# Kernel optimization log

Measured on AMD Instinct MI355X. Metric: run time of the kernel, lower is better.

The kernel has to match this reference:

```python
import jax, jax.numpy as jnp
import numpy as np

NUM_HEADS = 32
NUM_KV_HEADS = 8
HEAD_DIM = 128
ROPE_BASE = 10000.0


def rotate_half(x):
    half = x.shape[-1] // 2
    x1, x2 = x[..., :half], x[..., half:]
    return jnp.concatenate((-x2, x1), axis=-1)


def rope_cos_sin(position_ids, head_dim, dtype):
    # inv_freq: [head_dim/2]
    inv_freq = 1.0 / (ROPE_BASE ** (jnp.arange(0, head_dim, 2, dtype=jnp.float32) / head_dim))
    freqs = position_ids.astype(jnp.float32)[..., None] * inv_freq  # [B, S, hd/2]
    emb = jnp.concatenate((freqs, freqs), axis=-1)                  # [B, S, hd]
    # add head axis -> [B, 1, S, hd]
    return jnp.cos(emb)[:, None].astype(dtype), jnp.sin(emb)[:, None].astype(dtype)


def setup_inputs() -> dict:
    key = jax.random.key(0)
    k_x, k_q, k_k, k_v, k_o = jax.random.split(key, 5)
    B, S, H = 1, 2048, 4096
    w_scale = 0.02
    return {
        "hidden_states": jax.random.normal(k_x, (B, S, H), dtype=jnp.float32),
        "position_ids": jnp.broadcast_to(jnp.arange(S, dtype=jnp.int32), (B, S)),
        "Wq": jax.random.normal(k_q, (NUM_HEADS * HEAD_DIM, H), dtype=jnp.float32) * w_scale,
        "Wk": jax.random.normal(k_k, (NUM_KV_HEADS * HEAD_DIM, H), dtype=jnp.float32) * w_scale,
        "Wv": jax.random.normal(k_v, (NUM_KV_HEADS * HEAD_DIM, H), dtype=jnp.float32) * w_scale,
        "Wo": jax.random.normal(k_o, (H, NUM_HEADS * HEAD_DIM), dtype=jnp.float32) * w_scale,
    }


def reference(hidden_states, position_ids, Wq, Wk, Wv, Wo):
    B, S, H = hidden_states.shape
    n_rep = NUM_HEADS // NUM_KV_HEADS

    # projections (torch Linear: y = x @ W.T), reshape to [B, heads, S, hd]
    q = (hidden_states @ Wq.T).reshape(B, S, NUM_HEADS, HEAD_DIM).transpose(0, 2, 1, 3)
    k = (hidden_states @ Wk.T).reshape(B, S, NUM_KV_HEADS, HEAD_DIM).transpose(0, 2, 1, 3)
    v = (hidden_states @ Wv.T).reshape(B, S, NUM_KV_HEADS, HEAD_DIM).transpose(0, 2, 1, 3)

    cos, sin = rope_cos_sin(position_ids, HEAD_DIM, hidden_states.dtype)
    q = q * cos + rotate_half(q) * sin
    k = k * cos + rotate_half(k) * sin

    # repeat_kv: GQA expansion to [B, NUM_HEADS, S, hd]
    k = jnp.repeat(k, n_rep, axis=1)
    v = jnp.repeat(v, n_rep, axis=1)

    scale = 1.0 / jnp.sqrt(jnp.asarray(HEAD_DIM, dtype=hidden_states.dtype))
    scores = jnp.einsum('bhqd,bhkd->bhqk', q, k) * scale  # [B, H, S, S]

    # causal additive mask
    causal = jnp.tril(jnp.ones((S, S), dtype=bool))
    scores = jnp.where(causal[None, None], scores, jnp.finfo(scores.dtype).min)

    probs = jax.nn.softmax(scores, axis=-1)
    attn = jnp.einsum('bhqk,bhkd->bhqd', probs, v)         # [B, H, S, hd]
    attn = attn.transpose(0, 2, 1, 3).reshape(B, S, NUM_HEADS * HEAD_DIM)
    return attn @ Wo.T
```

## Files before the change

kernel.cpp:

```cpp
#include <hip/hip_runtime.h>
#include <hip/hip_bf16.h>
#include <stdint.h>

typedef __bf16 bf16;
typedef __attribute__((ext_vector_type(8))) __bf16 bf16x8;
typedef __attribute__((ext_vector_type(4))) __bf16 bf16x4;
typedef __attribute__((ext_vector_type(4))) float f32x4;
typedef __attribute__((ext_vector_type(16))) float f32x16;
typedef __attribute__((ext_vector_type(4))) unsigned int uint4v;

#define S_LEN 2048
#define HDIM  4096
#define NQH   32
#define NKVH  8
#define DHEAD 128
#define QKVN  6144
#define KOFF  4096
#define VOFF  5120
#define NSPLIT 4

__device__ __forceinline__ void gload_lds16(const bf16* g, bf16* l) {
  __builtin_amdgcn_global_load_lds(
      (const __attribute__((address_space(1))) unsigned int*)g,
      (__attribute__((address_space(3))) unsigned int*)l, 16, 0, 0);
}

__global__ __launch_bounds__(256) void cvt_f32_bf16(const float* __restrict__ in,
                                                    bf16* __restrict__ out, int n4) {
  int i = blockIdx.x * 256 + threadIdx.x;
  if (i >= n4) return;
  float4 v = ((const float4*)in)[i];
  bf16x4 ov = {(bf16)v.x, (bf16)v.y, (bf16)v.z, (bf16)v.w};
  *(bf16x4*)&out[(size_t)i * 4] = ov;
}

__global__ __launch_bounds__(256) void rope_table(const int* __restrict__ pos,
                                                  float* __restrict__ tab) {
  int idx = blockIdx.x * 256 + threadIdx.x;
  int i = idx & 63, s = idx >> 6;
  float p = (float)pos[s];
  float invf = powf(10000.0f, -(float)i * (1.0f / 64.0f));
  float ang = p * invf;
  tab[idx * 2]     = cosf(ang);
  tab[idx * 2 + 1] = sinf(ang);
}

__global__ __launch_bounds__(256) void rope_apply(bf16* __restrict__ QKV,
                                                  const float* __restrict__ tab) {
  int idx = blockIdx.x * 256 + threadIdx.x;
  int dp = idx & 63;
  int t = idx >> 6;
  int head = t % 40;
  int s = t / 40;
  float c  = tab[(s * 64 + dp) * 2];
  float sn = tab[(s * 64 + dp) * 2 + 1];
  size_t base = (size_t)s * QKVN + head * DHEAD;
  float x0 = (float)QKV[base + dp];
  float x1 = (float)QKV[base + 64 + dp];
  QKV[base + dp]      = (bf16)(x0 * c - x1 * sn);
  QKV[base + 64 + dp] = (bf16)(x1 * c + x0 * sn);
}

__global__ __launch_bounds__(256) void transpose_v(const bf16* __restrict__ QKV,
                                                   bf16* __restrict__ Vt) {
  __shared__ bf16 t[64][72];
  int tid = threadIdx.x;
  int bs = blockIdx.x * 64, bc = blockIdx.y * 64;
  int sl = tid >> 3, cb = (tid & 7) * 8;
#pragma unroll
  for (int ss = 0; ss < 64; ss += 32) {
    int s = sl + ss;
    *(bf16x8*)&t[s][cb] = *(const bf16x8*)&QKV[(size_t)(bs + s) * QKVN + VOFF + bc + cb];
  }
  __syncthreads();
  int cl = tid >> 3, sb = (tid & 7) * 8;
#pragma unroll
  for (int cc = 0; cc < 64; cc += 32) {
    int c = cl + cc;
    bf16x8 v;
#pragma unroll
    for (int k = 0; k < 8; ++k) v[k] = t[sb + k][c];
    *(bf16x8*)&Vt[(size_t)(bc + c) * S_LEN + bs + sb] = v;
  }
}

template <typename OutT>
__global__ __launch_bounds__(256) void gemm_bt(const bf16* __restrict__ A,
                                               const bf16* __restrict__ B,
                                               OutT* __restrict__ C,
                                               int M, int N, int K) {
  __shared__ bf16 At[128 * 64];
  __shared__ bf16 Bt[128 * 64];
  const int tid = threadIdx.x;
  const int w = tid >> 6, lane = tid & 63;
  const int r = lane & 15, g = lane >> 4;
  const int bm = blockIdx.y * 128, bn = blockIdx.x * 128;
  const int wm = (w >> 1) * 64, wn = (w & 1) * 64;
  f32x4 acc[4][4];
#pragma unroll
  for (int i = 0; i < 4; ++i)
#pragma unroll
    for (int j = 0; j < 4; ++j) acc[i][j] = (f32x4){0.f, 0.f, 0.f, 0.f};

  const int chunk0 = w * 256 + lane;

  for (int k0 = 0; k0 < K; k0 += 64) {
#pragma unroll
    for (int i = 0; i < 4; ++i) {
      int chunk = chunk0 + i * 64;
      int row = chunk >> 3, c8 = chunk & 7;
      int cs = ((c8 ^ (row & 7)) << 3) + k0;
      gload_lds16(&A[(size_t)(bm + row) * K + cs], &At[(w * 4 + i) * 512]);
      gload_lds16(&B[(size_t)(bn + row) * K + cs], &Bt[(w * 4 + i) * 512]);
    }
    __syncthreads();
#pragma unroll
    for (int ks = 0; ks < 2; ++ks) {
      bf16x8 af[4], bfr[4];
#pragma unroll
      for (int mi = 0; mi < 4; ++mi) {
        int row = wm + mi * 16 + r;
        af[mi] = *(const bf16x8*)&At[row * 64 + ((((ks << 2) + g) ^ (row & 7)) << 3)];
      }
#pragma unroll
      for (int nj = 0; nj < 4; ++nj) {
        int row = wn + nj * 16 + r;
        bfr[nj] = *(const bf16x8*)&Bt[row * 64 + ((((ks << 2) + g) ^ (row & 7)) << 3)];
      }
#pragma unroll
      for (int mi = 0; mi < 4; ++mi)
#pragma unroll
        for (int nj = 0; nj < 4; ++nj)
          acc[mi][nj] = __builtin_amdgcn_mfma_f32_16x16x32_bf16(af[mi], bfr[nj],
                                                                acc[mi][nj], 0, 0, 0);
    }
    __syncthreads();
  }
#pragma unroll
  for (int mi = 0; mi < 4; ++mi)
#pragma unroll
    for (int nj = 0; nj < 4; ++nj)
#pragma unroll
      for (int j = 0; j < 4; ++j) {
        int row = bm + wm + mi * 16 + g * 4 + j;
        int col = bn + wn + nj * 16 + r;
        C[(size_t)row * N + col] = (OutT)acc[mi][nj][j];
      }
}

__global__ __launch_bounds__(256) void attn_kernel(const bf16* __restrict__ QKV,
                                                   const bf16* __restrict__ Vt,
                                                   bf16* __restrict__ Opart,
                                                   float* __restrict__ Mpart,
                                                   float* __restrict__ Lpart) {
  __shared__ bf16 Kl[3][32 * 128];
  __shared__ bf16 Vl[3][128 * 32];
  const int tid = threadIdx.x;
  const int w = tid >> 6, lane = tid & 63;
  const int l31 = lane & 31, hi = lane >> 5;
  const int bx = blockIdx.x;
  const int kvh = bx & 7;
  const int rest = bx >> 3;
  const int s = rest & 3;
  const int qblk = 63 - (rest >> 2);
  const int h = kvh * 4 + w;
  const int q0 = qblk * 32;
  const int pid = (h * 64 + qblk) * NSPLIT + s;
  const float scale = 0.12751746f;

  const int nt = qblk + 1;
  const int t0 = (nt * s) >> 2;
  const int t1 = (nt * (s + 1)) >> 2;

  f32x16 o[4];
#pragma unroll
  for (int t = 0; t < 4; ++t)
#pragma unroll
    for (int r = 0; r < 16; ++r) o[t][r] = 0.f;
  float m_run = -1e30f, l_run = 0.f;

  auto stage = [&](int bufi, int kv0) {
#pragma unroll
    for (int ii = 0; ii < 2; ++ii) {
      int ins = w * 2 + ii;
      int hr = ins * 8 + (lane >> 3);
      int kvrow = hr >> 1, hK = hr & 1;
      int gk = ((lane & 7) ^ (kvrow & 7)) + 8 * hK;
      gload_lds16(&QKV[(size_t)(kv0 + kvrow) * QKVN + KOFF + kvh * DHEAD + gk * 8],
                  &Kl[bufi][ins * 512]);
      int pr = ins * 8 + (lane >> 3);
      int xv = (lane & 7) ^ (pr & 7);
      int dV = pr * 2 + (xv >> 2);
      gload_lds16(&Vt[(size_t)(kvh * DHEAD + dV) * S_LEN + kv0 + (xv & 3) * 8],
                  &Vl[bufi][ins * 512]);
    }
  };

  if (t0 < t1) {
    bf16x8 qf[8];
#pragma unroll
    for (int k8 = 0; k8 < 8; ++k8) {
      bf16x8 raw = *(const bf16x8*)&QKV[(size_t)(q0 + l31) * QKVN + h * DHEAD + k8 * 16 + hi * 8];
#pragma unroll
      for (int e = 0; e < 8; ++e) qf[k8][e] = (bf16)((float)raw[e] * scale);
    }

    int cur = t0 % 3;
    stage(cur, t0 * 32);
    if (t0 + 1 < t1) {
      stage(cur == 2 ? 0 : cur + 1, (t0 + 1) * 32);
      asm volatile("s_waitcnt vmcnt(4)" ::: "memory");
    } else {
      asm volatile("s_waitcnt vmcnt(0)" ::: "memory");
    }
    __builtin_amdgcn_s_barrier();
    asm volatile("" ::: "memory");

    for (int t = t0; t < t1; ++t) {
      if (t + 2 < t1) {
        int s2 = cur ? cur - 1 : 2;
        stage(s2, (t + 2) * 32);
      }

      f32x16 st;
#pragma unroll
      for (int r = 0; r < 16; ++r) st[r] = 0.f;
      __builtin_amdgcn_s_setprio(1);
#pragma unroll
      for (int k8 = 0; k8 < 8; ++k8) {
        int g = 2 * k8 + hi;
        bf16x8 kf = *(const bf16x8*)&Kl[cur][l31 * 128 + (g >> 3) * 64 +
                                             (((g & 7) ^ (l31 & 7)) << 3)];
        st = __builtin_amdgcn_mfma_f32_32x32x16_bf16(kf, qf[k8], st, 0, 0, 0);
      }
      __builtin_amdgcn_s_setprio(0);

      if (t == nt - 1) {
#pragma unroll
        for (int r = 0; r < 16; ++r) {
          int kvr = (r & 3) + 8 * (r >> 2) + 4 * hi;
          if (kvr > l31) st[r] = -1e30f;
        }
      }
      float pmax = st[0];
#pragma unroll
      for (int r = 1; r < 16; ++r) pmax = fmaxf(pmax, st[r]);
      pmax = fmaxf(pmax, __shfl_xor(pmax, 32));
      if (!__all(pmax - m_run <= 8.0f)) {
        float mnew = fmaxf(m_run, pmax);
        float corr = exp2f(m_run - mnew);
        m_run = mnew;
        l_run *= corr;
#pragma unroll
        for (int r = 0; r < 16; ++r) {
          float cr = __shfl(corr, (r & 3) + 8 * (r >> 2) + 4 * hi);
          o[0][r] *= cr; o[1][r] *= cr; o[2][r] *= cr; o[3][r] *= cr;
        }
      }
      float rs = 0.f;
#pragma unroll
      for (int r = 0; r < 16; ++r) { st[r] = exp2f(st[r] - m_run); rs += st[r]; }
      rs += __shfl_xor(rs, 32);
      l_run += rs;
      bf16x8 pf0, pf1;
      {
        unsigned int A0[4], X0[4];
#pragma unroll
        for (int j = 0; j < 4; ++j) {
          unsigned short lo = __builtin_bit_cast(unsigned short, (bf16)st[2 * j]);
          unsigned short hi16 = __builtin_bit_cast(unsigned short, (bf16)st[2 * j + 1]);
          A0[j] = (unsigned int)lo | ((unsigned int)hi16 << 16);
        }
#pragma unroll
        for (int j = 0; j < 4; ++j) X0[j] = __shfl_xor(A0[j], 32);
        uint4v w0v = {hi ? X0[2] : A0[0], hi ? X0[3] : A0[1],
                      hi ? A0[2] : X0[0], hi ? A0[3] : X0[1]};
        pf0 = __builtin_bit_cast(bf16x8, w0v);
      }
      {
        unsigned int A1[4], X1[4];
#pragma unroll
        for (int j = 0; j < 4; ++j) {
          unsigned short lo = __builtin_bit_cast(unsigned short, (bf16)st[8 + 2 * j]);
          unsigned short hi16 = __builtin_bit_cast(unsigned short, (bf16)st[9 + 2 * j]);
          A1[j] = (unsigned int)lo | ((unsigned int)hi16 << 16);
        }
#pragma unroll
        for (int j = 0; j < 4; ++j) X1[j] = __shfl_xor(A1[j], 32);
        uint4v w1v = {hi ? X1[2] : A1[0], hi ? X1[3] : A1[1],
                      hi ? A1[2] : X1[0], hi ? A1[3] : X1[1]};
        pf1 = __builtin_bit_cast(bf16x8, w1v);
      }
      __builtin_amdgcn_s_setprio(1);
#pragma unroll
      for (int tt = 0; tt < 4; ++tt) {
        int pr = tt * 16 + (l31 >> 1);
        int sb4 = (l31 & 1) << 2;
        bf16x8 v0 = *(const bf16x8*)&Vl[cur][pr * 64 + (((sb4 + hi) ^ (pr & 7)) << 3)];
        bf16x8 v1 = *(const bf16x8*)&Vl[cur][pr * 64 + (((sb4 + 2 + hi) ^ (pr & 7)) << 3)];
        o[tt] = __builtin_amdgcn_mfma_f32_32x32x16_bf16(pf0, v0, o[tt], 0, 0, 0);
        o[tt] = __builtin_amdgcn_mfma_f32_32x32x16_bf16(pf1, v1, o[tt], 0, 0, 0);
      }
      __builtin_amdgcn_s_setprio(0);

      if (t + 2 < t1) {
        asm volatile("s_waitcnt vmcnt(4)" ::: "memory");
      } else {
        asm volatile("s_waitcnt vmcnt(0)" ::: "memory");
      }
      __builtin_amdgcn_s_barrier();
      asm volatile("" ::: "memory");
      cur = (cur == 2) ? 0 : cur + 1;
    }
  }

  float linv = (l_run > 0.f) ? 1.0f / l_run : 0.f;
  if (hi == 0) {
    Mpart[pid * 32 + l31] = m_run;
    Lpart[pid * 32 + l31] = l_run;
  }
#pragma unroll
  for (int r = 0; r < 16; ++r) {
    int qloc = (r & 3) + 8 * (r >> 2) + 4 * hi;
    float li = __shfl(linv, qloc);
    size_t row = (size_t)pid * (32 * DHEAD) + (size_t)qloc * DHEAD;
#pragma unroll
    for (int t2 = 0; t2 < 4; ++t2)
      Opart[row + t2 * 32 + l31] = (bf16)(o[t2][r] * li);
  }
}

__global__ __launch_bounds__(256) void attn_merge(const bf16* __restrict__ Opart,
                                                  const float* __restrict__ Mpart,
                                                  const float* __restrict__ Lpart,
                                                  bf16* __restrict__ Oout) {
  const int bx = blockIdx.x;
  const int h = bx >> 6, qblk = bx & 63;
  const int tid = threadIdx.x;
  const int r = tid >> 3, cseg = (tid & 7) * 16;
  const int pid0 = bx * NSPLIT;
  float m[NSPLIT], l[NSPLIT];
  float M = -1e30f;
#pragma unroll
  for (int s = 0; s < NSPLIT; ++s) {
    m[s] = Mpart[(pid0 + s) * 32 + r];
    l[s] = Lpart[(pid0 + s) * 32 + r];
    M = fmaxf(M, m[s]);
  }
  float wsum = 0.f, wv[NSPLIT];
#pragma unroll
  for (int s = 0; s < NSPLIT; ++s) { wv[s] = l[s] * exp2f(m[s] - M); wsum += wv[s]; }
  float inv = 1.0f / wsum;
#pragma unroll
  for (int s = 0; s < NSPLIT; ++s) wv[s] *= inv;
  size_t dst = (size_t)(qblk * 32 + r) * HDIM + h * DHEAD + cseg;
#pragma unroll
  for (int half = 0; half < 2; ++half) {
    float acc[8];
#pragma unroll
    for (int e = 0; e < 8; ++e) acc[e] = 0.f;
#pragma unroll
    for (int s = 0; s < NSPLIT; ++s) {
      bf16x8 a = *(const bf16x8*)&Opart[(size_t)(pid0 + s) * (32 * DHEAD) +
                                        (size_t)r * DHEAD + cseg + half * 8];
#pragma unroll
      for (int e = 0; e < 8; ++e) acc[e] += wv[s] * (float)a[e];
    }
    bf16x8 out;
#pragma unroll
    for (int e = 0; e < 8; ++e) out[e] = (bf16)acc[e];
    *(bf16x8*)&Oout[dst + half * 8] = out;
  }
}

extern "C" void kernel_launch(void* const* d_in, const int* in_sizes, int n_in,
                              void* d_out, int out_size, void* d_ws, size_t ws_size,
                              hipStream_t stream) {
  const float* X   = (const float*)d_in[0];
  const int*   pos = (const int*)d_in[1];
  const float* Wq  = (const float*)d_in[2];
  const float* Wk  = (const float*)d_in[3];
  const float* Wv  = (const float*)d_in[4];
  const float* Wo  = (const float*)d_in[5];
  float* out = (float*)d_out;
  char* ws = (char*)d_ws;

  size_t off = 0;
  bf16* Xb    = (bf16*)(ws + off); off += (size_t)2048 * 4096 * 2;
  bf16* Wqkvb = (bf16*)(ws + off); off += (size_t)6144 * 4096 * 2;
  bf16* Wob   = (bf16*)(ws + off); off += (size_t)4096 * 4096 * 2;
  bf16* QKV   = (bf16*)(ws + off); off += (size_t)2048 * 6144 * 2;
  bf16* Vt    = (bf16*)(ws + off); off += (size_t)1024 * 2048 * 2;
  bf16* attnb = (bf16*)(ws + off); off += (size_t)2048 * 4096 * 2;
  float* tab  = (float*)(ws + off); off += (size_t)2048 * 64 * 2 * 4;
  float* Mpart = (float*)(ws + off); off += (size_t)8192 * 32 * 4;
  float* Lpart = (float*)(ws + off); off += (size_t)8192 * 32 * 4;

  bf16* Opart = (bf16*)Xb;

  cvt_f32_bf16<<<2048 * 4096 / 4 / 256, 256, 0, stream>>>(X, Xb, 2048 * 4096 / 4);
  cvt_f32_bf16<<<4096 * 4096 / 4 / 256, 256, 0, stream>>>(Wq, Wqkvb, 4096 * 4096 / 4);
  cvt_f32_bf16<<<1024 * 4096 / 4 / 256, 256, 0, stream>>>(Wk, Wqkvb + (size_t)4096 * 4096,
                                                          1024 * 4096 / 4);
  cvt_f32_bf16<<<1024 * 4096 / 4 / 256, 256, 0, stream>>>(Wv, Wqkvb + (size_t)5120 * 4096,
                                                          1024 * 4096 / 4);
  cvt_f32_bf16<<<4096 * 4096 / 4 / 256, 256, 0, stream>>>(Wo, Wob, 4096 * 4096 / 4);
  rope_table<<<2048 * 64 / 256, 256, 0, stream>>>(pos, tab);
  gemm_bt<bf16><<<dim3(QKVN / 128, 2048 / 128), 256, 0, stream>>>(Xb, Wqkvb, QKV,
                                                                  2048, QKVN, 4096);
  rope_apply<<<2048 * 40 * 64 / 256, 256, 0, stream>>>(QKV, tab);
  transpose_v<<<dim3(2048 / 64, 1024 / 64), 256, 0, stream>>>(QKV, Vt);
  attn_kernel<<<2048, 256, 0, stream>>>(QKV, Vt, Opart, Mpart, Lpart);
  attn_merge<<<2048, 256, 0, stream>>>(Opart, Mpart, Lpart, attnb);
  gemm_bt<float><<<dim3(4096 / 128, 2048 / 128), 256, 0, stream>>>(attnb, Wob, out,
                                                                   2048, 4096, 4096);
}
```

Baseline: 372.4 us.

## Replace GEMM with 256x256 double-buffered tiles, 8 waves, and XCD-aware swizzle

Both projection GEMMs move from 128x128 tiles with 4 waves to 256x256 tiles with 8 waves. The new kernel double-buffers LDS with async global-to-LDS prefetch of the next K slice, interleaved with MFMA phases and s_setprio hints. Block IDs are remapped so consecutive blocks spread across the 8 XCDs. Bigger tiles raise arithmetic intensity and the prefetch hides load latency. In exchange the grid is only 192 or 128 blocks for 256 CUs, which may underfill the GPU, and 128KB of LDS per block limits occupancy.

New measurement: 502.7 us. 1.35x slower.

```diff
diff --git a/kernel.cpp b/kernel.cpp
--- a/kernel.cpp
+++ b/kernel.cpp
@@ -85,65 +85,152 @@
 }
 
 template <typename OutT>
-__global__ __launch_bounds__(256) void gemm_bt(const bf16* __restrict__ A,
-                                               const bf16* __restrict__ B,
-                                               OutT* __restrict__ C,
-                                               int M, int N, int K) {
-  __shared__ bf16 At[128 * 64];
-  __shared__ bf16 Bt[128 * 64];
+__global__ __launch_bounds__(512, 2) void gemm_bt256(const bf16* __restrict__ A,
+                                                     const bf16* __restrict__ B,
+                                                     OutT* __restrict__ C,
+                                                     int M, int N, int K, int NX) {
+  __shared__ bf16 Al[2][256 * 64];
+  __shared__ bf16 Bl[2][256 * 64];
   const int tid = threadIdx.x;
   const int w = tid >> 6, lane = tid & 63;
   const int r = lane & 15, g = lane >> 4;
-  const int bm = blockIdx.y * 128, bn = blockIdx.x * 128;
-  const int wm = (w >> 1) * 64, wn = (w & 1) * 64;
-  f32x4 acc[4][4];
-#pragma unroll
-  for (int i = 0; i < 4; ++i)
-#pragma unroll
-    for (int j = 0; j < 4; ++j) acc[i][j] = (f32x4){0.f, 0.f, 0.f, 0.f};
-
-  const int chunk0 = w * 256 + lane;
-
-  for (int k0 = 0; k0 < K; k0 += 64) {
-#pragma unroll
-    for (int i = 0; i < 4; ++i) {
-      int chunk = chunk0 + i * 64;
-      int row = chunk >> 3, c8 = chunk & 7;
-      int cs = ((c8 ^ (row & 7)) << 3) + k0;
-      gload_lds16(&A[(size_t)(bm + row) * K + cs], &At[(w * 4 + i) * 512]);
-      gload_lds16(&B[(size_t)(bn + row) * K + cs], &Bt[(w * 4 + i) * 512]);
-    }
+  const int wr = w >> 2, wc = w & 3;
+  const int nwg = gridDim.x;
+  const int id = blockIdx.x;
+  const int q = nwg >> 3;
+  const int sw = (id & 7) * q + (id >> 3);
+  const int by = sw / NX, bx = sw - by * NX;
+  const int bm = by * 256, bn = bx * 256;
+
+  f32x4 acc[8][4];
+#pragma unroll
+  for (int mi = 0; mi < 8; ++mi)
+#pragma unroll
+    for (int nj = 0; nj < 4; ++nj) acc[mi][nj] = (f32x4){0.f, 0.f, 0.f, 0.f};
+
+  int rowS[4], colS[4];
+#pragma unroll
+  for (int i = 0; i < 4; ++i) {
+    int chunk = (i * 8 + w) * 64 + lane;
+    rowS[i] = chunk >> 3;
+    colS[i] = ((chunk & 7) ^ (rowS[i] & 7)) << 3;
+  }
+
+  const int NT = K >> 6;
+#pragma unroll
+  for (int i = 0; i < 4; ++i) {
+    gload_lds16(&A[(size_t)(bm + rowS[i]) * K + colS[i]], &Al[0][(i * 8 + w) * 512]);
+    gload_lds16(&B[(size_t)(bn + rowS[i]) * K + colS[i]], &Bl[0][(i * 8 + w) * 512]);
+  }
+  __syncthreads();
+
+  for (int t = 0; t < NT; ++t) {
+    const int cur = t & 1;
+    const bf16* Ac = Al[cur];
+    const bf16* Bc = Bl[cur];
+    bf16* An = Al[cur ^ 1];
+    bf16* Bn = Bl[cur ^ 1];
+    const int kn = (t + 1) << 6;
+    const bool pre = (t + 1 < NT);
+    bf16x8 af[4], bfr[4];
+
+    if (pre) {
+#pragma unroll
+      for (int i = 0; i < 4; ++i)
+        gload_lds16(&A[(size_t)(bm + rowS[i]) * K + kn + colS[i]], &An[(i * 8 + w) * 512]);
+    }
+#pragma unroll
+    for (int mi = 0; mi < 4; ++mi) {
+      int row = wr * 128 + mi * 16 + r;
+      af[mi] = *(const bf16x8*)&Ac[row * 64 + ((g ^ (row & 7)) << 3)];
+    }
+#pragma unroll
+    for (int nj = 0; nj < 4; ++nj) {
+      int row = wc * 64 + nj * 16 + r;
+      bfr[nj] = *(const bf16x8*)&Bc[row * 64 + ((g ^ (row & 7)) << 3)];
+    }
+    __builtin_amdgcn_s_barrier();
+    asm volatile("s_waitcnt lgkmcnt(0)" ::: "memory");
+    __builtin_amdgcn_s_setprio(1);
+#pragma unroll
+    for (int mi = 0; mi < 4; ++mi)
+#pragma unroll
+      for (int nj = 0; nj < 4; ++nj)
+        acc[mi][nj] = __builtin_amdgcn_mfma_f32_16x16x32_bf16(af[mi], bfr[nj],
+                                                              acc[mi][nj], 0, 0, 0);
+    __builtin_amdgcn_s_setprio(0);
+    __builtin_amdgcn_s_barrier();
+
+    if (pre) {
+#pragma unroll
+      for (int i = 0; i < 4; ++i)
+        gload_lds16(&B[(size_t)(bn + rowS[i]) * K + kn + colS[i]], &Bn[(i * 8 + w) * 512]);
+    }
+#pragma unroll
+    for (int mi = 0; mi < 4; ++mi) {
+      int row = wr * 128 + (mi + 4) * 16 + r;
+      af[mi] = *(const bf16x8*)&Ac[row * 64 + ((g ^ (row & 7)) << 3)];
+    }
+    __builtin_amdgcn_s_barrier();
+    asm volatile("s_waitcnt lgkmcnt(0)" ::: "memory");
+    __builtin_amdgcn_s_setprio(1);
+#pragma unroll
+    for (int mi = 0; mi < 4; ++mi)
+#pragma unroll
+      for (int nj = 0; nj < 4; ++nj)
+        acc[mi + 4][nj] = __builtin_amdgcn_mfma_f32_16x16x32_bf16(af[mi], bfr[nj],
+                                                                  acc[mi + 4][nj], 0, 0, 0);
+    __builtin_amdgcn_s_setprio(0);
+    __builtin_amdgcn_s_barrier();
+
+#pragma unroll
+    for (int mi = 0; mi < 4; ++mi) {
+      int row = wr * 128 + mi * 16 + r;
+      af[mi] = *(const bf16x8*)&Ac[row * 64 + (((4 + g) ^ (row & 7)) << 3)];
+    }
+#pragma unroll
+    for (int nj = 0; nj < 4; ++nj) {
+      int row = wc * 64 + nj * 16 + r;
+      bfr[nj] = *(const bf16x8*)&Bc[row * 64 + (((4 + g) ^ (row & 7)) << 3)];
+    }
+    __builtin_amdgcn_s_barrier();
+    asm volatile("s_waitcnt lgkmcnt(0)" ::: "memory");
+    __builtin_amdgcn_s_setprio(1);
+#pragma unroll
+    for (int mi = 0; mi < 4; ++mi)
+#pragma unroll
+      for (int nj = 0; nj < 4; ++nj)
+        acc[mi][nj] = __builtin_amdgcn_mfma_f32_16x16x32_bf16(af[mi], bfr[nj],
+                                                              acc[mi][nj], 0, 0, 0);
+    __builtin_amdgcn_s_setprio(0);
+    __builtin_amdgcn_s_barrier();
+
+#pragma unroll
+    for (int mi = 0; mi < 4; ++mi) {
+      int row = wr * 128 + (mi + 4) * 16 + r;
+      af[mi] = *(const bf16x8*)&Ac[row * 64 + (((4 + g) ^ (row & 7)) << 3)];
+    }
+    __builtin_amdgcn_s_barrier();
+    asm volatile("s_waitcnt lgkmcnt(0)" ::: "memory");
+    __builtin_amdgcn_s_setprio(1);
+#pragma unroll
+    for (int mi = 0; mi < 4; ++mi)
+#pragma unroll
+      for (int nj = 0; nj < 4; ++nj)
+        acc[mi + 4][nj] = __builtin_amdgcn_mfma_f32_16x16x32_bf16(af[mi], bfr[nj],
+                                                                  acc[mi + 4][nj], 0, 0, 0);
+    __builtin_amdgcn_s_setprio(0);
     __syncthreads();
-#pragma unroll
-    for (int ks = 0; ks < 2; ++ks) {
-      bf16x8 af[4], bfr[4];
-#pragma unroll
-      for (int mi = 0; mi < 4; ++mi) {
-        int row = wm + mi * 16 + r;
-        af[mi] = *(const bf16x8*)&At[row * 64 + ((((ks << 2) + g) ^ (row & 7)) << 3)];
-      }
-#pragma unroll
-      for (int nj = 0; nj < 4; ++nj) {
-        int row = wn + nj * 16 + r;
-        bfr[nj] = *(const bf16x8*)&Bt[row * 64 + ((((ks << 2) + g) ^ (row & 7)) << 3)];
-      }
-#pragma unroll
-      for (int mi = 0; mi < 4; ++mi)
-#pragma unroll
-        for (int nj = 0; nj < 4; ++nj)
-          acc[mi][nj] = __builtin_amdgcn_mfma_f32_16x16x32_bf16(af[mi], bfr[nj],
-                                                                acc[mi][nj], 0, 0, 0);
-    }
-    __syncthreads();
-  }
-#pragma unroll
-  for (int mi = 0; mi < 4; ++mi)
+  }
+
+#pragma unroll
+  for (int mi = 0; mi < 8; ++mi)
 #pragma unroll
     for (int nj = 0; nj < 4; ++nj)
 #pragma unroll
       for (int j = 0; j < 4; ++j) {
-        int row = bm + wm + mi * 16 + g * 4 + j;
-        int col = bn + wn + nj * 16 + r;
+        int row = bm + wr * 128 + mi * 16 + g * 4 + j;
+        int col = bn + wc * 64 + nj * 16 + r;
         C[(size_t)row * N + col] = (OutT)acc[mi][nj][j];
       }
 }
@@ -406,12 +493,10 @@
                                                           1024 * 4096 / 4);
   cvt_f32_bf16<<<4096 * 4096 / 4 / 256, 256, 0, stream>>>(Wo, Wob, 4096 * 4096 / 4);
   rope_table<<<2048 * 64 / 256, 256, 0, stream>>>(pos, tab);
-  gemm_bt<bf16><<<dim3(QKVN / 128, 2048 / 128), 256, 0, stream>>>(Xb, Wqkvb, QKV,
-                                                                  2048, QKVN, 4096);
+  gemm_bt256<bf16><<<dim3(192), 512, 0, stream>>>(Xb, Wqkvb, QKV, 2048, QKVN, 4096, 24);
   rope_apply<<<2048 * 40 * 64 / 256, 256, 0, stream>>>(QKV, tab);
   transpose_v<<<dim3(2048 / 64, 1024 / 64), 256, 0, stream>>>(QKV, Vt);
   attn_kernel<<<2048, 256, 0, stream>>>(QKV, Vt, Opart, Mpart, Lpart);
   attn_merge<<<2048, 256, 0, stream>>>(Opart, Mpart, Lpart, attnb);
-  gemm_bt<float><<<dim3(4096 / 128, 2048 / 128), 256, 0, stream>>>(attnb, Wob, out,
-                                                                   2048, 4096, 4096);
-}
+  gemm_bt256<float><<<dim3(128), 512, 0, stream>>>(attnb, Wob, out, 2048, 4096, 4096, 16);
+}
```

## Replace GEMM with 8-wave, 4-stage pipelined kernel and XCD-aware tile mapping

Applied to the files above, without the earlier changes.

Swaps the 128x128 single-buffered GEMM for a templated 512-thread kernel with larger tiles (256x256 for QKV, 256x128 for the output projection). Global-to-LDS loads run in a four-slot ring, two k-steps ahead, with explicit vmcnt waits. Compute is split into two MFMA phases interleaved with LDS fragment loads and raised with setprio. Block IDs are remapped so tiles that share data land on the same XCD, aiming for better L2 reuse. The hand-written waitcnt/barrier scheme is fragile, and larger tiles mean fewer blocks (192/256) on a 256-CU device.

New measurement: 465.3 us. 24.9% more time.

```diff
diff --git a/kernel.cpp b/kernel.cpp
--- a/kernel.cpp
+++ b/kernel.cpp
@@ -84,66 +84,130 @@
   }
 }
 
-template <typename OutT>
-__global__ __launch_bounds__(256) void gemm_bt(const bf16* __restrict__ A,
-                                               const bf16* __restrict__ B,
-                                               OutT* __restrict__ C,
-                                               int M, int N, int K) {
-  __shared__ bf16 At[128 * 64];
-  __shared__ bf16 Bt[128 * 64];
+template <typename OutT, int BM, int BN, int WM, int WN, int XR, int XC, int XCX>
+__global__ __launch_bounds__(512, 2) void gemm8p(const bf16* __restrict__ A,
+                                                 const bf16* __restrict__ B,
+                                                 OutT* __restrict__ C,
+                                                 int M, int N, int K) {
+  constexpr int PM = BM / WM, PN = BN / WN;
+  constexpr int MI = PM / 16, NJ = PN / 16;
+  constexpr int MIH = MI / 2;
+  constexpr int LA = BM / 128, LB = BN / 128;
+  __shared__ bf16 Abuf[4][BM * 32];
+  __shared__ bf16 Bbuf[4][BN * 32];
   const int tid = threadIdx.x;
   const int w = tid >> 6, lane = tid & 63;
   const int r = lane & 15, g = lane >> 4;
-  const int bm = blockIdx.y * 128, bn = blockIdx.x * 128;
-  const int wm = (w >> 1) * 64, wn = (w & 1) * 64;
-  f32x4 acc[4][4];
-#pragma unroll
-  for (int i = 0; i < 4; ++i)
-#pragma unroll
-    for (int j = 0; j < 4; ++j) acc[i][j] = (f32x4){0.f, 0.f, 0.f, 0.f};
-
-  const int chunk0 = w * 256 + lane;
-
-  for (int k0 = 0; k0 < K; k0 += 64) {
-#pragma unroll
-    for (int i = 0; i < 4; ++i) {
-      int chunk = chunk0 + i * 64;
-      int row = chunk >> 3, c8 = chunk & 7;
-      int cs = ((c8 ^ (row & 7)) << 3) + k0;
-      gload_lds16(&A[(size_t)(bm + row) * K + cs], &At[(w * 4 + i) * 512]);
-      gload_lds16(&B[(size_t)(bn + row) * K + cs], &Bt[(w * 4 + i) * 512]);
-    }
-    __syncthreads();
-#pragma unroll
-    for (int ks = 0; ks < 2; ++ks) {
-      bf16x8 af[4], bfr[4];
-#pragma unroll
-      for (int mi = 0; mi < 4; ++mi) {
-        int row = wm + mi * 16 + r;
-        af[mi] = *(const bf16x8*)&At[row * 64 + ((((ks << 2) + g) ^ (row & 7)) << 3)];
-      }
-#pragma unroll
-      for (int nj = 0; nj < 4; ++nj) {
-        int row = wn + nj * 16 + r;
-        bfr[nj] = *(const bf16x8*)&Bt[row * 64 + ((((ks << 2) + g) ^ (row & 7)) << 3)];
-      }
-#pragma unroll
-      for (int mi = 0; mi < 4; ++mi)
-#pragma unroll
-        for (int nj = 0; nj < 4; ++nj)
-          acc[mi][nj] = __builtin_amdgcn_mfma_f32_16x16x32_bf16(af[mi], bfr[nj],
-                                                                acc[mi][nj], 0, 0, 0);
-    }
-    __syncthreads();
-  }
-#pragma unroll
-  for (int mi = 0; mi < 4; ++mi)
-#pragma unroll
-    for (int nj = 0; nj < 4; ++nj)
+  const int wr = w / WN, wc = w % WN;
+  const int id = blockIdx.x;
+  const int xcd = id & 7, o = id >> 3;
+  const int by = (xcd / XCX) * XR + o / XC;
+  const int bx = (xcd % XCX) * XC + o % XC;
+  const int bm = by * BM, bn = bx * BN;
+
+  f32x4 acc[MI][NJ];
+#pragma unroll
+  for (int mi = 0; mi < MI; ++mi)
+#pragma unroll
+    for (int nj = 0; nj < NJ; ++nj) acc[mi][nj] = (f32x4){0.f, 0.f, 0.f, 0.f};
+
+  auto stageA = [&](int slot, int k0) {
+#pragma unroll
+    for (int j = 0; j < LA; ++j) {
+      int cid = (j * 8 + w) * 64 + lane;
+      int row = cid >> 2, c = cid & 3;
+      int sw = (row ^ (row >> 2)) & 3;
+      gload_lds16(&A[(size_t)(bm + row) * K + k0 + ((c ^ sw) << 3)],
+                  &Abuf[slot][(j * 8 + w) * 512]);
+    }
+  };
+  auto stageB = [&](int slot, int k0) {
+#pragma unroll
+    for (int j = 0; j < LB; ++j) {
+      int cid = (j * 8 + w) * 64 + lane;
+      int row = cid >> 2, c = cid & 3;
+      int sw = (row ^ (row >> 2)) & 3;
+      gload_lds16(&B[(size_t)(bn + row) * K + k0 + ((c ^ sw) << 3)],
+                  &Bbuf[slot][(j * 8 + w) * 512]);
+    }
+  };
+
+  const int NT = K >> 5;
+  stageA(0, 0);  stageB(0, 0);
+  stageA(1, 32); stageB(1, 32);
+  if constexpr (LA + LB == 4) asm volatile("s_waitcnt vmcnt(4)" ::: "memory");
+  else                        asm volatile("s_waitcnt vmcnt(3)" ::: "memory");
+  __builtin_amdgcn_s_barrier();
+  asm volatile("" ::: "memory");
+
+  for (int t = 0; t < NT; ++t) {
+    const int slot = t & 3;
+    const bf16* Ac = Abuf[slot];
+    const bf16* Bc = Bbuf[slot];
+    const bool pre = (t + 2 < NT);
+    if (pre) { stageA((t + 2) & 3, (t + 2) << 5); stageB((t + 2) & 3, (t + 2) << 5); }
+
+    bf16x8 af[MIH], af2[MIH], bfr[NJ];
+#pragma unroll
+    for (int mi = 0; mi < MIH; ++mi) {
+      int row = wr * PM + mi * 16 + r;
+      int sw = (row ^ (row >> 2)) & 3;
+      af[mi] = *(const bf16x8*)&Ac[row * 32 + ((g ^ sw) << 3)];
+    }
+#pragma unroll
+    for (int nj = 0; nj < NJ; ++nj) {
+      int row = wc * PN + nj * 16 + r;
+      int sw = (row ^ (row >> 2)) & 3;
+      bfr[nj] = *(const bf16x8*)&Bc[row * 32 + ((g ^ sw) << 3)];
+    }
+    __builtin_amdgcn_s_barrier();
+    asm volatile("s_waitcnt lgkmcnt(0)" ::: "memory");
+    __builtin_amdgcn_s_setprio(1);
+#pragma unroll
+    for (int mi = 0; mi < MIH; ++mi)
+#pragma unroll
+      for (int nj = 0; nj < NJ; ++nj)
+        acc[mi][nj] = __builtin_amdgcn_mfma_f32_16x16x32_bf16(af[mi], bfr[nj],
+                                                              acc[mi][nj], 0, 0, 0);
+    __builtin_amdgcn_s_setprio(0);
+    __builtin_amdgcn_s_barrier();
+    asm volatile("" ::: "memory");
+
+#pragma unroll
+    for (int mi = 0; mi < MIH; ++mi) {
+      int row = wr * PM + (MIH + mi) * 16 + r;
+      int sw = (row ^ (row >> 2)) & 3;
+      af2[mi] = *(const bf16x8*)&Ac[row * 32 + ((g ^ sw) << 3)];
+    }
+    __builtin_amdgcn_s_barrier();
+    asm volatile("s_waitcnt lgkmcnt(0)" ::: "memory");
+    __builtin_amdgcn_s_setprio(1);
+#pragma unroll
+    for (int mi = 0; mi < MIH; ++mi)
+#pragma unroll
+      for (int nj = 0; nj < NJ; ++nj)
+        acc[MIH + mi][nj] = __builtin_amdgcn_mfma_f32_16x16x32_bf16(af2[mi], bfr[nj],
+                                                                    acc[MIH + mi][nj], 0, 0, 0);
+    __builtin_amdgcn_s_setprio(0);
+
+    if (pre) {
+      if constexpr (LA + LB == 4) asm volatile("s_waitcnt vmcnt(4)" ::: "memory");
+      else                        asm volatile("s_waitcnt vmcnt(3)" ::: "memory");
+    } else {
+      asm volatile("s_waitcnt vmcnt(0)" ::: "memory");
+    }
+    __builtin_amdgcn_s_barrier();
+    asm volatile("" ::: "memory");
+  }
+
+#pragma unroll
+  for (int mi = 0; mi < MI; ++mi)
+#pragma unroll
+    for (int nj = 0; nj < NJ; ++nj)
 #pragma unroll
       for (int j = 0; j < 4; ++j) {
-        int row = bm + wm + mi * 16 + g * 4 + j;
-        int col = bn + wn + nj * 16 + r;
+        int row = bm + wr * PM + mi * 16 + g * 4 + j;
+        int col = bn + wc * PN + nj * 16 + r;
         C[(size_t)row * N + col] = (OutT)acc[mi][nj][j];
       }
 }
@@ -406,12 +470,12 @@
                                                           1024 * 4096 / 4);
   cvt_f32_bf16<<<4096 * 4096 / 4 / 256, 256, 0, stream>>>(Wo, Wob, 4096 * 4096 / 4);
   rope_table<<<2048 * 64 / 256, 256, 0, stream>>>(pos, tab);
-  gemm_bt<bf16><<<dim3(QKVN / 128, 2048 / 128), 256, 0, stream>>>(Xb, Wqkvb, QKV,
-                                                                  2048, QKVN, 4096);
+  gemm8p<bf16, 256, 256, 2, 4, 4, 6, 4><<<192, 512, 0, stream>>>(Xb, Wqkvb, QKV,
+                                                                 2048, QKVN, 4096);
   rope_apply<<<2048 * 40 * 64 / 256, 256, 0, stream>>>(QKV, tab);
   transpose_v<<<dim3(2048 / 64, 1024 / 64), 256, 0, stream>>>(QKV, Vt);
   attn_kernel<<<2048, 256, 0, stream>>>(QKV, Vt, Opart, Mpart, Lpart);
   attn_merge<<<2048, 256, 0, stream>>>(Opart, Mpart, Lpart, attnb);
-  gemm_bt<float><<<dim3(4096 / 128, 2048 / 128), 256, 0, stream>>>(attnb, Wob, out,
-                                                                   2048, 4096, 4096);
-}
+  gemm8p<float, 256, 128, 4, 2, 4, 8, 4><<<256, 512, 0, stream>>>(attnb, Wob, out,
+                                                                  2048, 4096, 4096);
+}
```

## Replace GEMM with pipelined 512-thread kernel using triple-buffered A and XCD-aware tiling

Applied to the files above, without the earlier changes.

Replaces the simple 128x128 single-buffered GEMM with a 512-thread kernel that uses larger N tiles (384 for QKV, 256 for output), triple-buffered A and double-buffered B in LDS. Global-to-LDS prefetches for the next tiles are interleaved with the MFMA phases, and s_setprio raises priority around the MFMA blocks. Block indices are remapped so neighbouring tiles land on the same XCD, improving L2 reuse. The aim is to hide memory latency and cut the barrier stalls of the old load-sync-compute loop, at the cost of more LDS use and delicate vmcnt accounting.

Result: no change. 371.5 us (-0.2%).

```diff
diff --git a/kernel.cpp b/kernel.cpp
--- a/kernel.cpp
+++ b/kernel.cpp
@@ -84,66 +84,113 @@
   }
 }
 
-template <typename OutT>
-__global__ __launch_bounds__(256) void gemm_bt(const bf16* __restrict__ A,
-                                               const bf16* __restrict__ B,
-                                               OutT* __restrict__ C,
-                                               int M, int N, int K) {
-  __shared__ bf16 At[128 * 64];
-  __shared__ bf16 Bt[128 * 64];
+template <typename OutT, int BN>
+__global__ __launch_bounds__(512, 2) void gemm_ph(const bf16* __restrict__ A,
+                                                  const bf16* __restrict__ B,
+                                                  OutT* __restrict__ C,
+                                                  int M, int N, int K) {
+  constexpr int NJ = BN / 64;
+  constexpr int NJH = NJ / 2;
+  constexpr int LB = BN / 64;
+  constexpr int WCW = BN / 4;
+  __shared__ bf16 Al[3][128 * 64];
+  __shared__ bf16 Bl[2][BN * 64];
   const int tid = threadIdx.x;
   const int w = tid >> 6, lane = tid & 63;
   const int r = lane & 15, g = lane >> 4;
-  const int bm = blockIdx.y * 128, bn = blockIdx.x * 128;
-  const int wm = (w >> 1) * 64, wn = (w & 1) * 64;
-  f32x4 acc[4][4];
-#pragma unroll
-  for (int i = 0; i < 4; ++i)
-#pragma unroll
-    for (int j = 0; j < 4; ++j) acc[i][j] = (f32x4){0.f, 0.f, 0.f, 0.f};
-
-  const int chunk0 = w * 256 + lane;
-
-  for (int k0 = 0; k0 < K; k0 += 64) {
-#pragma unroll
-    for (int i = 0; i < 4; ++i) {
-      int chunk = chunk0 + i * 64;
-      int row = chunk >> 3, c8 = chunk & 7;
-      int cs = ((c8 ^ (row & 7)) << 3) + k0;
-      gload_lds16(&A[(size_t)(bm + row) * K + cs], &At[(w * 4 + i) * 512]);
-      gload_lds16(&B[(size_t)(bn + row) * K + cs], &Bt[(w * 4 + i) * 512]);
-    }
-    __syncthreads();
-#pragma unroll
-    for (int ks = 0; ks < 2; ++ks) {
-      bf16x8 af[4], bfr[4];
-#pragma unroll
-      for (int mi = 0; mi < 4; ++mi) {
-        int row = wm + mi * 16 + r;
-        af[mi] = *(const bf16x8*)&At[row * 64 + ((((ks << 2) + g) ^ (row & 7)) << 3)];
-      }
-#pragma unroll
-      for (int nj = 0; nj < 4; ++nj) {
-        int row = wn + nj * 16 + r;
-        bfr[nj] = *(const bf16x8*)&Bt[row * 64 + ((((ks << 2) + g) ^ (row & 7)) << 3)];
-      }
+  const int wr = w >> 2, wc = w & 3;
+  const int id = blockIdx.x;
+  const int xcd = id & 7, o = id >> 3;
+  const int by = o >> 1, bx = xcd * 2 + (o & 1);
+  const int bm = by * 128, bn = bx * BN;
+
+  f32x4 acc[4][NJ];
+#pragma unroll
+  for (int mi = 0; mi < 4; ++mi)
+#pragma unroll
+    for (int nj = 0; nj < NJ; ++nj) acc[mi][nj] = (f32x4){0.f, 0.f, 0.f, 0.f};
+
+  auto stageA = [&](int slot, int k0) {
+#pragma unroll
+    for (int j = 0; j < 2; ++j) {
+      int chunk = (j * 8 + w) * 64 + lane;
+      int row = chunk >> 3, c = chunk & 7;
+      gload_lds16(&A[(size_t)(bm + row) * K + k0 + ((c ^ (row & 7)) << 3)],
+                  &Al[slot][(j * 8 + w) * 512]);
+    }
+  };
+  auto stageB = [&](int buf, int k0, int i0, int i1) {
+#pragma unroll
+    for (int i = 0; i < LB; ++i) {
+      if (i < i0 || i >= i1) continue;
+      int chunk = (i * 8 + w) * 64 + lane;
+      int row = chunk >> 3, c = chunk & 7;
+      gload_lds16(&B[(size_t)(bn + row) * K + k0 + ((c ^ (row & 7)) << 3)],
+                  &Bl[buf][(i * 8 + w) * 512]);
+    }
+  };
+
+  const int NT = K >> 6;
+  stageA(0, 0);
+  stageB(0, 0, 0, LB);
+  stageA(1, 64);
+  asm volatile("s_waitcnt vmcnt(2)" ::: "memory");
+  __builtin_amdgcn_s_barrier();
+  asm volatile("" ::: "memory");
+
+  for (int t = 0; t < NT; ++t) {
+    const bf16* Ac = Al[t % 3];
+    const bf16* Bc = Bl[t & 1];
+    const bool p1 = (t + 1 < NT), p2 = (t + 2 < NT);
+    const int kn = (t + 1) << 6;
+    bf16x8 af[4], bfr[NJH];
+
+#pragma unroll
+    for (int p = 0; p < 4; ++p) {
+      const int ks = p >> 1, njh = p & 1;
+      if (njh == 0) {
+#pragma unroll
+        for (int mi = 0; mi < 4; ++mi) {
+          int row = wr * 64 + mi * 16 + r;
+          af[mi] = *(const bf16x8*)&Ac[row * 64 + (((ks * 4 + g) ^ (row & 7)) << 3)];
+        }
+      }
+#pragma unroll
+      for (int nj = 0; nj < NJH; ++nj) {
+        int row = wc * WCW + (njh * NJH + nj) * 16 + r;
+        bfr[nj] = *(const bf16x8*)&Bc[row * 64 + (((ks * 4 + g) ^ (row & 7)) << 3)];
+      }
+      if (p == 0 && p1) stageB((t + 1) & 1, kn, 0, 2);
+      if (p == 1 && p1) stageB((t + 1) & 1, kn, 2, 4);
+      if (p == 2 && p1) stageB((t + 1) & 1, kn, 4, LB);
+      if (p == 3 && p2) stageA((t + 2) % 3, (t + 2) << 6);
+      __builtin_amdgcn_s_barrier();
+      asm volatile("s_waitcnt lgkmcnt(0)" ::: "memory");
+      __builtin_amdgcn_s_setprio(1);
 #pragma unroll
       for (int mi = 0; mi < 4; ++mi)
 #pragma unroll
-        for (int nj = 0; nj < 4; ++nj)
-          acc[mi][nj] = __builtin_amdgcn_mfma_f32_16x16x32_bf16(af[mi], bfr[nj],
-                                                                acc[mi][nj], 0, 0, 0);
-    }
-    __syncthreads();
-  }
+        for (int nj = 0; nj < NJH; ++nj)
+          acc[mi][njh * NJH + nj] = __builtin_amdgcn_mfma_f32_16x16x32_bf16(
+              af[mi], bfr[nj], acc[mi][njh * NJH + nj], 0, 0, 0);
+      __builtin_amdgcn_s_setprio(0);
+      __builtin_amdgcn_s_barrier();
+      asm volatile("" ::: "memory");
+    }
+    if (p2) asm volatile("s_waitcnt vmcnt(2)" ::: "memory");
+    else    asm volatile("s_waitcnt vmcnt(0)" ::: "memory");
+    __builtin_amdgcn_s_barrier();
+    asm volatile("" ::: "memory");
+  }
+
 #pragma unroll
   for (int mi = 0; mi < 4; ++mi)
 #pragma unroll
-    for (int nj = 0; nj < 4; ++nj)
+    for (int nj = 0; nj < NJ; ++nj)
 #pragma unroll
       for (int j = 0; j < 4; ++j) {
-        int row = bm + wm + mi * 16 + g * 4 + j;
-        int col = bn + wn + nj * 16 + r;
+        int row = bm + wr * 64 + mi * 16 + g * 4 + j;
+        int col = bn + wc * WCW + nj * 16 + r;
         C[(size_t)row * N + col] = (OutT)acc[mi][nj][j];
       }
 }
@@ -406,12 +453,10 @@
                                                           1024 * 4096 / 4);
   cvt_f32_bf16<<<4096 * 4096 / 4 / 256, 256, 0, stream>>>(Wo, Wob, 4096 * 4096 / 4);
   rope_table<<<2048 * 64 / 256, 256, 0, stream>>>(pos, tab);
-  gemm_bt<bf16><<<dim3(QKVN / 128, 2048 / 128), 256, 0, stream>>>(Xb, Wqkvb, QKV,
-                                                                  2048, QKVN, 4096);
+  gemm_ph<bf16, 384><<<256, 512, 0, stream>>>(Xb, Wqkvb, QKV, 2048, QKVN, 4096);
   rope_apply<<<2048 * 40 * 64 / 256, 256, 0, stream>>>(QKV, tab);
   transpose_v<<<dim3(2048 / 64, 1024 / 64), 256, 0, stream>>>(QKV, Vt);
   attn_kernel<<<2048, 256, 0, stream>>>(QKV, Vt, Opart, Mpart, Lpart);
   attn_merge<<<2048, 256, 0, stream>>>(Opart, Mpart, Lpart, attnb);
-  gemm_bt<float><<<dim3(4096 / 128, 2048 / 128), 256, 0, stream>>>(attnb, Wob, out,
-                                                                   2048, 4096, 4096);
-}
+  gemm_ph<float, 256><<<256, 512, 0, stream>>>(attnb, Wob, out, 2048, 4096, 4096);
+}
```
